# Kernel tuning notes

Hardware: AMD Instinct MI355X
Metric: run time of the kernel (lower is better)

## Reference

```python
import jax, jax.numpy as jnp
import numpy as np

THETA = 10000.0


def apply_rope(x, positions, theta=THETA):
    # x: [B, H, N, D], positions: [1, N] or [B, N]
    D = x.shape[-1]
    inv_freq = 1.0 / (theta ** (jnp.arange(0, D, 2, dtype=jnp.float32) / D))  # [D/2]
    ang = positions.astype(jnp.float32)[:, None, :, None] * inv_freq  # [B_or_1, 1, N, D/2]
    cos, sin = jnp.cos(ang), jnp.sin(ang)
    x1 = x[..., 0::2]
    x2 = x[..., 1::2]
    r1 = x1 * cos - x2 * sin
    r2 = x1 * sin + x2 * cos
    # interleave back to [..., D]
    return jnp.stack([r1, r2], axis=-1).reshape(x.shape)


def setup_inputs() -> dict:
    key = jax.random.key(0)
    ks = jax.random.split(key, 5)
    B, N, d_model = 2, 2048, 1024
    s = 1.0 / np.sqrt(d_model)
    return {
        "x": jax.random.normal(ks[0], (B, N, d_model), dtype=jnp.float32),
        "Wq": jax.random.normal(ks[1], (d_model, d_model), dtype=jnp.float32) * s,
        "Wk": jax.random.normal(ks[2], (d_model, d_model), dtype=jnp.float32) * s,
        "Wv": jax.random.normal(ks[3], (d_model, d_model), dtype=jnp.float32) * s,
        "Wo": jax.random.normal(ks[4], (d_model, d_model), dtype=jnp.float32) * s,
        "token_positions": jnp.arange(N, dtype=jnp.int32)[None, :],
    }


def reference(x, Wq, Wk, Wv, Wo, token_positions):
    B, N, d_model = x.shape
    H = 16
    D = d_model // H
    # projections: out = x @ W.T  (einsum '... i, j i -> ... j')
    def proj(W):
        y = jnp.einsum('bni,ji->bnj', x, W)
        return y.reshape(B, N, H, D).transpose(0, 2, 1, 3)  # [B,H,N,D]
    q, k, v = proj(Wq), proj(Wk), proj(Wv)
    q = apply_rope(q, token_positions)
    k = apply_rope(k, token_positions)
    scale = 1.0 / jnp.sqrt(jnp.asarray(D, dtype=x.dtype))
    scores = jnp.einsum('bhid,bhjd->bhij', q, k) * scale  # [B,H,N,N]
    causal = jnp.tril(jnp.ones((N, N), dtype=bool))
    scores = jnp.where(causal[None, None], scores, -jnp.inf)
    w = jax.nn.softmax(scores, axis=-1)
    o = jnp.einsum('bhij,bhjd->bhid', w, v)  # [B,H,N,D]
    o = o.transpose(0, 2, 1, 3).reshape(B, N, d_model)
    return jnp.einsum('bni,ji->bnj', o, Wo)
```

## Files before the change

kernel.cpp:

```cpp
#include <hip/hip_runtime.h>

#define DMODEL 1024
#define NSEQ   2048
#define BSZ    2
#define NH     16
#define HD     64
#define MROWS  (BSZ*NSEQ)

using short8 = __attribute__((ext_vector_type(8))) short;
using f32x4  = __attribute__((ext_vector_type(4))) float;

__device__ __forceinline__ short f2b(float f) {
  unsigned u = __builtin_bit_cast(unsigned, f);
  u += 0x7fffu + ((u >> 16) & 1u);
  return (short)(u >> 16);
}

__device__ __forceinline__ void load_lds16(const void* g, void* l) {
  __builtin_amdgcn_global_load_lds((const __attribute__((address_space(1))) unsigned int*)g,
                                   (__attribute__((address_space(3))) unsigned int*)l,
                                   16, 0, 0);
}

__global__ void cvt_all(const float* __restrict__ x,  const float* __restrict__ Wq,
                        const float* __restrict__ Wk, const float* __restrict__ Wv,
                        const float* __restrict__ Wo, const int* __restrict__ pos,
                        short* __restrict__ xb,  short* __restrict__ wqb,
                        short* __restrict__ wkb, short* __restrict__ wvb,
                        short* __restrict__ wob, float* __restrict__ cs) {
  const int NX  = (BSZ * NSEQ * DMODEL) / 4;
  const int NW  = (DMODEL * DMODEL) / 4;
  const int NCV = NX + 4 * NW;
  const int TOT = NCV + NSEQ * 32;
  for (int i = blockIdx.x * blockDim.x + threadIdx.x; i < TOT; i += gridDim.x * blockDim.x) {
    if (i < NCV) {
      const float* src; short* dst; int off;
      if (i < NX) { src = x; dst = xb; off = i; }
      else {
        int j = i - NX; int s = j >> 18; off = j & (NW - 1);
        src = (s == 0) ? Wq : (s == 1) ? Wk : (s == 2) ? Wv : Wo;
        dst = (s == 0) ? wqb : (s == 1) ? wkb : (s == 2) ? wvb : wob;
      }
      float4 v = reinterpret_cast<const float4*>(src)[off];
      short4 r;
      r.x = f2b(v.x); r.y = f2b(v.y); r.z = f2b(v.z); r.w = f2b(v.w);
      reinterpret_cast<short4*>(dst)[off] = r;
    } else {
      int idx = i - NCV;
      int n = idx >> 5, p = idx & 31;
      float inv = powf(10000.0f, -(float)(2 * p) / 64.0f);
      float ang = (float)pos[n] * inv;
      cs[idx * 2]     = cosf(ang);
      cs[idx * 2 + 1] = sinf(ang);
    }
  }
}

__global__ __launch_bounds__(512, 1) void gemm_qkv3(
    const short* __restrict__ xb,
    const short* __restrict__ wq, const short* __restrict__ wk, const short* __restrict__ wv,
    const float* __restrict__ cs,
    short* __restrict__ qb, short* __restrict__ kb, short* __restrict__ vt) {
  __shared__ short Al[2][128 * 64];
  __shared__ short Bl[2][3][128 * 64];

  const int t   = threadIdx.x;
  const int l   = t & 63;
  const int wid = t >> 6;
  const int wr  = (wid >> 2) * 64;
  const int wc  = (wid & 3) * 32;

  const int id = blockIdx.x;
  const int bx = id & 31;
  const int np = id >> 5;
  const int arow0 = bx * 128;
  const int bcol0 = np * 128;

  const int tr = t >> 3;
  const int c8 = (t & 7) ^ ((t >> 3) & 7);
  const short* W3[3] = {wq, wk, wv};

  auto STAGE = [&](int kt, int buf) {
#pragma unroll
    for (int h = 0; h < 2; ++h)
      load_lds16(xb + (size_t)(arow0 + h * 64 + tr) * DMODEL + kt * 64 + c8 * 8,
                 &Al[buf][h * 4096 + wid * 512]);
#pragma unroll
    for (int p = 0; p < 3; ++p)
#pragma unroll
      for (int h = 0; h < 2; ++h)
        load_lds16(W3[p] + (size_t)(bcol0 + h * 64 + tr) * DMODEL + kt * 64 + c8 * 8,
                   &Bl[buf][p][h * 4096 + wid * 512]);
  };

  f32x4 acc[3][4][2];
#pragma unroll
  for (int p = 0; p < 3; ++p)
#pragma unroll
    for (int mi = 0; mi < 4; ++mi)
#pragma unroll
      for (int ni = 0; ni < 2; ++ni) acc[p][mi][ni] = f32x4{0.f, 0.f, 0.f, 0.f};

  const int lr  = l & 15;
  const int lcb = (l >> 4) << 4;

  STAGE(0, 0);
  int cur = 0;

  for (int kt = 0; kt < DMODEL / 64; ++kt) {
    if (kt + 1 < DMODEL / 64) {
      STAGE(kt + 1, cur ^ 1);
      asm volatile("s_waitcnt vmcnt(8)" ::: "memory");
    } else {
      asm volatile("s_waitcnt vmcnt(0)" ::: "memory");
    }
    asm volatile("s_barrier" ::: "memory");

    const char* Ab = reinterpret_cast<const char*>(&Al[cur][0]);
#pragma unroll
    for (int ks = 0; ks < 2; ++ks) {
      const int cb = ks * 64 + lcb;
      short8 af[4];
#pragma unroll
      for (int mi = 0; mi < 4; ++mi) {
        int r = wr + mi * 16 + lr;
        af[mi] = *reinterpret_cast<const short8*>(Ab + r * 128 + (cb ^ ((r & 7) << 4)));
      }
#pragma unroll
      for (int p = 0; p < 3; ++p) {
        const char* Bb = reinterpret_cast<const char*>(&Bl[cur][p][0]);
        short8 bf[2];
#pragma unroll
        for (int ni = 0; ni < 2; ++ni) {
          int r = wc + ni * 16 + lr;
          bf[ni] = *reinterpret_cast<const short8*>(Bb + r * 128 + (cb ^ ((r & 7) << 4)));
        }
#pragma unroll
        for (int mi = 0; mi < 4; ++mi)
#pragma unroll
          for (int ni = 0; ni < 2; ++ni)
            acc[p][mi][ni] = __builtin_amdgcn_mfma_f32_16x16x32_bf16(af[mi], bf[ni], acc[p][mi][ni], 0, 0, 0);
      }
    }
    asm volatile("s_barrier" ::: "memory");
    cur ^= 1;
  }

#pragma unroll
  for (int p = 0; p < 3; ++p) {
#pragma unroll
    for (int mi = 0; mi < 4; ++mi) {
#pragma unroll
      for (int ni = 0; ni < 2; ++ni) {
#pragma unroll
        for (int r = 0; r < 4; ++r) {
          float v = acc[p][mi][ni][r];
          int m = arow0 + wr + mi * 16 + ((l >> 4) << 2) + r;
          int j = bcol0 + wc + ni * 16 + (l & 15);
          int n = m & (NSEQ - 1);
          int b = m >> 11;
          int h = j >> 6, d = j & 63, pp = d >> 1;
          float pv = __shfl_xor(v, 1);
          if (p < 2) {
            float c = cs[(n * 32 + pp) * 2];
            float s = cs[(n * 32 + pp) * 2 + 1];
            float res = (d & 1) ? (pv * s + v * c) : (v * c - pv * s);
            if (p == 0) res *= 0.180336880f;
            short* dst = (p == 0) ? qb : kb;
            dst[(((size_t)(b * NH + h)) * NSEQ + n) * HD + d] = f2b(res);
          } else {
            vt[(((size_t)(b * NH + h)) * HD + d) * NSEQ + n] = f2b(v);
          }
        }
      }
    }
  }
}

__device__ __forceinline__ void gemm_core(const short* __restrict__ A,
                                          const short* __restrict__ Bw,
                                          int arow0, int bcol0,
                                          short* As, short* Bs,
                                          f32x4 (&acc)[4][4]) {
  const int t = threadIdx.x;
  const int l = t & 63;
  const int w = t >> 6;
  const int wr = (w >> 1) * 64;
  const int wc = (w & 1) * 64;
  const int srow = t >> 3;
  const int c8   = (t & 7) ^ (srow & 7);

#pragma unroll
  for (int mi = 0; mi < 4; ++mi)
#pragma unroll
    for (int ni = 0; ni < 4; ++ni) acc[mi][ni] = f32x4{0.f, 0.f, 0.f, 0.f};

  auto STAGE = [&](int kt, int buf) {
#pragma unroll
    for (int is = 0; is < 4; ++is) {
      int row = srow + is * 32;
      load_lds16(A  + (size_t)(arow0 + row) * DMODEL + kt * 64 + c8 * 8,
                 As + buf * 8192 + w * 512 + is * 2048);
      load_lds16(Bw + (size_t)(bcol0 + row) * DMODEL + kt * 64 + c8 * 8,
                 Bs + buf * 8192 + w * 512 + is * 2048);
    }
  };

  STAGE(0, 0);
  int cur = 0;

  for (int kt = 0; kt < DMODEL / 64; ++kt) {
    if (kt + 1 < DMODEL / 64) {
      STAGE(kt + 1, cur ^ 1);
      asm volatile("s_waitcnt vmcnt(8)" ::: "memory");
    } else {
      asm volatile("s_waitcnt vmcnt(0)" ::: "memory");
    }
    asm volatile("s_barrier" ::: "memory");

    const char* Ab = reinterpret_cast<const char*>(As + cur * 8192);
    const char* Bb = reinterpret_cast<const char*>(Bs + cur * 8192);
#pragma unroll
    for (int ks = 0; ks < 2; ++ks) {
      short8 af[4], bf[4];
      const int cb = ks * 64 + ((l >> 4) * 16);
#pragma unroll
      for (int mi = 0; mi < 4; ++mi) {
        int rr = wr + mi * 16 + (l & 15);
        af[mi] = *reinterpret_cast<const short8*>(Ab + rr * 128 + (cb ^ ((rr & 7) << 4)));
      }
#pragma unroll
      for (int ni = 0; ni < 4; ++ni) {
        int rr = wc + ni * 16 + (l & 15);
        bf[ni] = *reinterpret_cast<const short8*>(Bb + rr * 128 + (cb ^ ((rr & 7) << 4)));
      }
#pragma unroll
      for (int mi = 0; mi < 4; ++mi)
#pragma unroll
        for (int ni = 0; ni < 4; ++ni)
          acc[mi][ni] = __builtin_amdgcn_mfma_f32_16x16x32_bf16(af[mi], bf[ni], acc[mi][ni], 0, 0, 0);
    }
    asm volatile("s_barrier" ::: "memory");
    cur ^= 1;
  }
}

__global__ __launch_bounds__(256) void gemm_out(
    const short* __restrict__ ob, const short* __restrict__ wo, float* __restrict__ out) {
  __shared__ short As[2 * 128 * 64];
  __shared__ short Bs[2 * 128 * 64];
  const int t = threadIdx.x;
  const int l = t & 63;
  const int w = t >> 6;
  const int wr = (w >> 1) * 64;
  const int wc = (w & 1) * 64;
  const int arow0 = blockIdx.x * 128;
  const int bcol0 = blockIdx.y * 128;

  f32x4 acc[4][4];
  gemm_core(ob, wo, arow0, bcol0, As, Bs, acc);

#pragma unroll
  for (int mi = 0; mi < 4; ++mi) {
#pragma unroll
    for (int ni = 0; ni < 4; ++ni) {
#pragma unroll
      for (int r = 0; r < 4; ++r) {
        int m = arow0 + wr + mi * 16 + ((l >> 4) << 2) + r;
        int j = bcol0 + wc + ni * 16 + (l & 15);
        out[(size_t)m * DMODEL + j] = acc[mi][ni][r];
      }
    }
  }
}

__global__ __launch_bounds__(512, 1) void attn(
    const short* __restrict__ qb, const short* __restrict__ kb,
    const short* __restrict__ vt, short* __restrict__ ob) {
  __shared__ short Ks[2][128 * 64];
  __shared__ short Vs[2][64 * 128];
  __shared__ short Ps[8][16 * 128];
  const int t = threadIdx.x;
  const int l = t & 63;
  const int w = t >> 6;
  const int id  = blockIdx.x;
  const int xcd = id & 7;
  const int bh  = xcd + 8 * (id >> 6);
  const int qy  = (id >> 3) & 7;
  const short* Q  = qb + (size_t)bh * NSEQ * HD;
  const short* Kg = kb + (size_t)bh * NSEQ * HD;
  const short* Vg = vt + (size_t)bh * HD * NSEQ;
  const int b = bh >> 4, h = bh & 15;

  const int trk = t >> 3;
  const int ck  = (t & 7) ^ ((t >> 3) & 7);
  const int trv = t >> 4;
  const int cv  = (t & 15) ^ ((t >> 4) & 15);
  const int irow = (l >> 4) << 2;
  const short8 ones = {(short)0x3F80, (short)0x3F80, (short)0x3F80, (short)0x3F80,
                       (short)0x3F80, (short)0x3F80, (short)0x3F80, (short)0x3F80};

  auto STAGEA = [&](int tile, int buf) {
    int j0 = tile * 128;
#pragma unroll
    for (int is = 0; is < 2; ++is) {
      load_lds16(Kg + (size_t)(j0 + trk + is * 64) * HD + ck * 8,
                 &Ks[buf][is * 4096 + w * 512]);
      load_lds16(Vg + (size_t)(trv + is * 32) * NSEQ + j0 + cv * 8,
                 &Vs[buf][is * 4096 + w * 512]);
    }
  };

  int cur = 0;
  for (int pass = 0; pass < 2; ++pass) {
    const int qt = pass ? (15 - qy) : qy;
    const int q0 = qt * 128;
    const int nt = qt + 1;

    STAGEA(0, cur);

    short8 qf[2];
    {
      int qrow = q0 + w * 16 + (l & 15);
#pragma unroll
      for (int ks = 0; ks < 2; ++ks)
        qf[ks] = *reinterpret_cast<const short8*>(Q + (size_t)qrow * HD + ks * 32 + (l >> 4) * 8);
    }

    f32x4 ao[4];
#pragma unroll
    for (int dt = 0; dt < 4; ++dt) ao[dt] = f32x4{0.f, 0.f, 0.f, 0.f};
    f32x4 accl = f32x4{0.f, 0.f, 0.f, 0.f};

    for (int tile = 0; tile < nt; ++tile) {
      if (tile + 1 < nt) {
        STAGEA(tile + 1, cur ^ 1);
        asm volatile("s_waitcnt vmcnt(4)" ::: "memory");
      } else {
        asm volatile("s_waitcnt vmcnt(0)" ::: "memory");
      }
      asm volatile("s_barrier" ::: "memory");

      const char* Kb = reinterpret_cast<const char*>(&Ks[cur][0]);
      const char* Vb = reinterpret_cast<const char*>(&Vs[cur][0]);

      f32x4 sc[8];
#pragma unroll
      for (int jt = 0; jt < 8; ++jt) sc[jt] = f32x4{0.f, 0.f, 0.f, 0.f};
#pragma unroll
      for (int ks = 0; ks < 2; ++ks) {
        const int cb = ks * 64 + ((l >> 4) * 16);
#pragma unroll
        for (int jt = 0; jt < 8; ++jt) {
          int kr = jt * 16 + (l & 15);
          short8 kf = *reinterpret_cast<const short8*>(Kb + kr * 128 + (cb ^ ((kr & 7) << 4)));
          sc[jt] = __builtin_amdgcn_mfma_f32_16x16x32_bf16(qf[ks], kf, sc[jt], 0, 0, 0);
        }
      }

      if (tile == nt - 1) {
        const int j0 = tile * 128;
#pragma unroll
        for (int jt = 0; jt < 8; ++jt)
#pragma unroll
          for (int r = 0; r < 4; ++r) {
            int i_g = q0 + w * 16 + irow + r;
            int j_g = j0 + jt * 16 + (l & 15);
            if (j_g > i_g) sc[jt][r] = -1e30f;
          }
      }

#pragma unroll
      for (int jt = 0; jt < 8; ++jt) {
#pragma unroll
        for (int r = 0; r < 4; ++r) {
          float p = __builtin_amdgcn_exp2f(sc[jt][r]);
          int i = irow + r;
          int jj = jt * 16 + (l & 15);
          Ps[w][i * 128 + (jj ^ ((i & 15) << 3))] =
              (short)(__builtin_bit_cast(unsigned, p) >> 16);
        }
      }

#pragma unroll
      for (int ks2 = 0; ks2 < 4; ++ks2) {
        const int cb = ks2 * 64 + ((l >> 4) * 16);
        int pr = l & 15;
        short8 pf = *reinterpret_cast<const short8*>(
            reinterpret_cast<const char*>(&Ps[w][0]) + pr * 256 + (cb ^ ((pr & 15) << 4)));
        accl = __builtin_amdgcn_mfma_f32_16x16x32_bf16(pf, ones, accl, 0, 0, 0);
#pragma unroll
        for (int dt = 0; dt < 4; ++dt) {
          int vr = dt * 16 + (l & 15);
          short8 vf = *reinterpret_cast<const short8*>(Vb + vr * 256 + (cb ^ ((vr & 15) << 4)));
          ao[dt] = __builtin_amdgcn_mfma_f32_16x16x32_bf16(pf, vf, ao[dt], 0, 0, 0);
        }
      }
      asm volatile("s_barrier" ::: "memory");
      cur ^= 1;
    }

#pragma unroll
    for (int dt = 0; dt < 4; ++dt) {
#pragma unroll
      for (int r = 0; r < 4; ++r) {
        int n = q0 + w * 16 + irow + r;
        int col = h * 64 + dt * 16 + (l & 15);
        ob[((size_t)b * NSEQ + n) * DMODEL + col] = f2b(ao[dt][r] / accl[r]);
      }
    }
  }
}

extern "C" void kernel_launch(void* const* d_in, const int* in_sizes, int n_in,
                              void* d_out, int out_size, void* d_ws, size_t ws_size,
                              hipStream_t stream) {
  const float* x  = (const float*)d_in[0];
  const float* Wq = (const float*)d_in[1];
  const float* Wk = (const float*)d_in[2];
  const float* Wv = (const float*)d_in[3];
  const float* Wo = (const float*)d_in[4];
  const int*   pos = (const int*)d_in[5];
  float* out = (float*)d_out;
  char* ws = (char*)d_ws;

  short* xb  = (short*)(ws);
  short* wqb = (short*)(ws + ((size_t)8  << 20));
  short* wkb = (short*)(ws + ((size_t)10 << 20));
  short* wvb = (short*)(ws + ((size_t)12 << 20));
  short* wob = (short*)(ws + ((size_t)14 << 20));
  short* qb  = (short*)(ws + ((size_t)16 << 20));
  short* kb  = (short*)(ws + ((size_t)24 << 20));
  short* vt  = (short*)(ws + ((size_t)32 << 20));
  short* ob  = (short*)(ws + ((size_t)40 << 20));
  float* cs  = (float*)(ws + ((size_t)48 << 20));

  cvt_all<<<2048, 256, 0, stream>>>(x, Wq, Wk, Wv, Wo, pos, xb, wqb, wkb, wvb, wob, cs);
  gemm_qkv3<<<256, 512, 0, stream>>>(xb, wqb, wkb, wvb, cs, qb, kb, vt);
  attn<<<256, 512, 0, stream>>>(qb, kb, vt, ob);
  gemm_out<<<dim3(32, 8), 256, 0, stream>>>(ob, wob, out);
}
```

Baseline: 102.8 us.

## Split attention key tile across wave groups with 32-row query fragments and LDS reduction

Each wave now handles 32 query rows against one 64-key half of every 128-key tile, instead of 16 rows against the full tile. Each K and V fragment loaded from LDS therefore feeds two MFMAs, which cuts LDS read traffic per MFMA. The two key-half groups combine their partial output and row-sum accumulators through LDS at the end of each pass, reusing the K/V buffers as scratch. The cost is more registers per wave, an extra reduction barrier, and one more barrier before staging each pass.

New measurement: 103.2 us. Within noise of the previous version (+0.3%).

```diff
diff --git a/kernel.cpp b/kernel.cpp
--- a/kernel.cpp
+++ b/kernel.cpp
@@ -279,10 +279,12 @@
     const short* __restrict__ vt, short* __restrict__ ob) {
   __shared__ short Ks[2][128 * 64];
   __shared__ short Vs[2][64 * 128];
-  __shared__ short Ps[8][16 * 128];
+  __shared__ short Ps[8][32 * 64];
   const int t = threadIdx.x;
   const int l = t & 63;
   const int w = t >> 6;
+  const int qs = w & 3;
+  const int g  = w >> 2;
   const int id  = blockIdx.x;
   const int xcd = id & 7;
   const int bh  = xcd + 8 * (id >> 6);
@@ -317,20 +319,26 @@
     const int q0 = qt * 128;
     const int nt = qt + 1;
 
+    asm volatile("s_barrier" ::: "memory");
     STAGEA(0, cur);
 
-    short8 qf[2];
+    short8 qf[2][2];
     {
-      int qrow = q0 + w * 16 + (l & 15);
-#pragma unroll
-      for (int ks = 0; ks < 2; ++ks)
-        qf[ks] = *reinterpret_cast<const short8*>(Q + (size_t)qrow * HD + ks * 32 + (l >> 4) * 8);
-    }
-
-    f32x4 ao[4];
-#pragma unroll
-    for (int dt = 0; dt < 4; ++dt) ao[dt] = f32x4{0.f, 0.f, 0.f, 0.f};
-    f32x4 accl = f32x4{0.f, 0.f, 0.f, 0.f};
+      int qr0 = q0 + qs * 32;
+#pragma unroll
+      for (int mi = 0; mi < 2; ++mi)
+#pragma unroll
+        for (int ks = 0; ks < 2; ++ks)
+          qf[mi][ks] = *reinterpret_cast<const short8*>(
+              Q + (size_t)(qr0 + mi * 16 + (l & 15)) * HD + ks * 32 + (l >> 4) * 8);
+    }
+
+    f32x4 ao[2][4];
+#pragma unroll
+    for (int mi = 0; mi < 2; ++mi)
+#pragma unroll
+      for (int dt = 0; dt < 4; ++dt) ao[mi][dt] = f32x4{0.f, 0.f, 0.f, 0.f};
+    f32x4 accl[2] = {f32x4{0.f, 0.f, 0.f, 0.f}, f32x4{0.f, 0.f, 0.f, 0.f}};
 
     for (int tile = 0; tile < nt; ++tile) {
       if (tile + 1 < nt) {
@@ -344,70 +352,113 @@
       const char* Kb = reinterpret_cast<const char*>(&Ks[cur][0]);
       const char* Vb = reinterpret_cast<const char*>(&Vs[cur][0]);
 
-      f32x4 sc[8];
-#pragma unroll
-      for (int jt = 0; jt < 8; ++jt) sc[jt] = f32x4{0.f, 0.f, 0.f, 0.f};
+      f32x4 sc[4][2];
+#pragma unroll
+      for (int jt = 0; jt < 4; ++jt)
+#pragma unroll
+        for (int mi = 0; mi < 2; ++mi) sc[jt][mi] = f32x4{0.f, 0.f, 0.f, 0.f};
 #pragma unroll
       for (int ks = 0; ks < 2; ++ks) {
         const int cb = ks * 64 + ((l >> 4) * 16);
 #pragma unroll
-        for (int jt = 0; jt < 8; ++jt) {
-          int kr = jt * 16 + (l & 15);
+        for (int jt = 0; jt < 4; ++jt) {
+          int kr = g * 64 + jt * 16 + (l & 15);
           short8 kf = *reinterpret_cast<const short8*>(Kb + kr * 128 + (cb ^ ((kr & 7) << 4)));
-          sc[jt] = __builtin_amdgcn_mfma_f32_16x16x32_bf16(qf[ks], kf, sc[jt], 0, 0, 0);
+#pragma unroll
+          for (int mi = 0; mi < 2; ++mi)
+            sc[jt][mi] = __builtin_amdgcn_mfma_f32_16x16x32_bf16(qf[mi][ks], kf, sc[jt][mi], 0, 0, 0);
         }
       }
 
       if (tile == nt - 1) {
-        const int j0 = tile * 128;
-#pragma unroll
-        for (int jt = 0; jt < 8; ++jt)
+        const int j0 = tile * 128 + g * 64;
+#pragma unroll
+        for (int jt = 0; jt < 4; ++jt)
+#pragma unroll
+          for (int mi = 0; mi < 2; ++mi)
+#pragma unroll
+            for (int r = 0; r < 4; ++r) {
+              int i_g = q0 + qs * 32 + mi * 16 + irow + r;
+              int j_g = j0 + jt * 16 + (l & 15);
+              if (j_g > i_g) sc[jt][mi][r] = -1e30f;
+            }
+      }
+
+#pragma unroll
+      for (int jt = 0; jt < 4; ++jt) {
+#pragma unroll
+        for (int mi = 0; mi < 2; ++mi)
 #pragma unroll
           for (int r = 0; r < 4; ++r) {
-            int i_g = q0 + w * 16 + irow + r;
-            int j_g = j0 + jt * 16 + (l & 15);
-            if (j_g > i_g) sc[jt][r] = -1e30f;
+            float p = __builtin_amdgcn_exp2f(sc[jt][mi][r]);
+            int i = mi * 16 + irow + r;
+            int jj = jt * 16 + (l & 15);
+            Ps[w][i * 64 + (jj ^ ((i & 7) << 3))] =
+                (short)(__builtin_bit_cast(unsigned, p) >> 16);
           }
       }
 
 #pragma unroll
-      for (int jt = 0; jt < 8; ++jt) {
-#pragma unroll
-        for (int r = 0; r < 4; ++r) {
-          float p = __builtin_amdgcn_exp2f(sc[jt][r]);
-          int i = irow + r;
-          int jj = jt * 16 + (l & 15);
-          Ps[w][i * 128 + (jj ^ ((i & 15) << 3))] =
-              (short)(__builtin_bit_cast(unsigned, p) >> 16);
-        }
-      }
-
-#pragma unroll
-      for (int ks2 = 0; ks2 < 4; ++ks2) {
+      for (int ks2 = 0; ks2 < 2; ++ks2) {
         const int cb = ks2 * 64 + ((l >> 4) * 16);
-        int pr = l & 15;
-        short8 pf = *reinterpret_cast<const short8*>(
-            reinterpret_cast<const char*>(&Ps[w][0]) + pr * 256 + (cb ^ ((pr & 15) << 4)));
-        accl = __builtin_amdgcn_mfma_f32_16x16x32_bf16(pf, ones, accl, 0, 0, 0);
-#pragma unroll
-        for (int dt = 0; dt < 4; ++dt) {
-          int vr = dt * 16 + (l & 15);
-          short8 vf = *reinterpret_cast<const short8*>(Vb + vr * 256 + (cb ^ ((vr & 15) << 4)));
-          ao[dt] = __builtin_amdgcn_mfma_f32_16x16x32_bf16(pf, vf, ao[dt], 0, 0, 0);
+#pragma unroll
+        for (int mi = 0; mi < 2; ++mi) {
+          int pr = mi * 16 + (l & 15);
+          short8 pf = *reinterpret_cast<const short8*>(
+              reinterpret_cast<const char*>(&Ps[w][0]) + pr * 128 + (cb ^ ((pr & 7) << 4)));
+          accl[mi] = __builtin_amdgcn_mfma_f32_16x16x32_bf16(pf, ones, accl[mi], 0, 0, 0);
+#pragma unroll
+          for (int dt = 0; dt < 4; ++dt) {
+            int vr = dt * 16 + (l & 15);
+            short8 vf = *reinterpret_cast<const short8*>(
+                Vb + vr * 256 + ((g * 128 + cb) ^ ((vr & 15) << 4)));
+            ao[mi][dt] = __builtin_amdgcn_mfma_f32_16x16x32_bf16(pf, vf, ao[mi][dt], 0, 0, 0);
+          }
         }
       }
       asm volatile("s_barrier" ::: "memory");
       cur ^= 1;
     }
 
-#pragma unroll
-    for (int dt = 0; dt < 4; ++dt) {
-#pragma unroll
-      for (int r = 0; r < 4; ++r) {
-        int n = q0 + w * 16 + irow + r;
-        int col = h * 64 + dt * 16 + (l & 15);
-        ob[((size_t)b * NSEQ + n) * DMODEL + col] = f2b(ao[dt][r] / accl[r]);
-      }
+    float* Opart = reinterpret_cast<float*>(&Ks[0][0]);
+    float* Apart = reinterpret_cast<float*>(&Vs[0][0]);
+    if (g == 1) {
+#pragma unroll
+      for (int mi = 0; mi < 2; ++mi) {
+#pragma unroll
+        for (int dt = 0; dt < 4; ++dt)
+#pragma unroll
+          for (int r = 0; r < 4; ++r)
+            Opart[qs * 2048 + (mi * 16 + irow + r) * 64 + dt * 16 + (l & 15)] = ao[mi][dt][r];
+        if ((l & 15) == 0)
+#pragma unroll
+          for (int r = 0; r < 4; ++r)
+            Apart[qs * 32 + mi * 16 + irow + r] = accl[mi][r];
+      }
+    }
+    asm volatile("s_barrier" ::: "memory");
+    if (g == 0) {
+#pragma unroll
+      for (int mi = 0; mi < 2; ++mi) {
+#pragma unroll
+        for (int dt = 0; dt < 4; ++dt)
+#pragma unroll
+          for (int r = 0; r < 4; ++r)
+            ao[mi][dt][r] += Opart[qs * 2048 + (mi * 16 + irow + r) * 64 + dt * 16 + (l & 15)];
+#pragma unroll
+        for (int r = 0; r < 4; ++r)
+          accl[mi][r] += Apart[qs * 32 + mi * 16 + irow + r];
+      }
+#pragma unroll
+      for (int mi = 0; mi < 2; ++mi)
+#pragma unroll
+        for (int dt = 0; dt < 4; ++dt)
+#pragma unroll
+          for (int r = 0; r < 4; ++r) {
+            int n = q0 + qs * 32 + mi * 16 + irow + r;
+            int col = h * 64 + dt * 16 + (l & 15);
+            ob[((size_t)b * NSEQ + n) * DMODEL + col] = f2b(ao[mi][dt][r] / accl[mi][r]);
+          }
     }
   }
 }
```
